# Optimization experiments

Hardware: AMD Instinct MI355X
Metric: run time of the kernel (lower is better)

## Reference

```python
import jax, jax.numpy as jnp
import numpy as np


def setup_inputs() -> dict:
    key = jax.random.key(0)
    ks = jax.random.split(key, 8)
    B, L, d_model = 2, 4096, 1024
    d_inner, d_state, d_conv, dt_rank = 2048, 16, 4, 64
    f = jnp.float32
    g = lambda k, shape, scale: jax.random.normal(k, shape, dtype=f) * scale
    # dt bias init: inverse-softplus of dt ~ U[log 1e-3, log 1e-1] (as in Mamba)
    dt = jnp.exp(jax.random.uniform(ks[5], (d_inner,), f) * (np.log(0.1) - np.log(0.001)) + np.log(0.001))
    dt = jnp.clip(dt, 1e-4, None)
    inv_dt = dt + jnp.log(-jnp.expm1(-dt))
    A_log = jnp.log(jnp.broadcast_to(jnp.arange(1, d_state + 1, dtype=f), (d_inner, d_state)))
    return {
        "hidden_states": jax.random.normal(ks[0], (B, L, d_model), f),
        "in_proj_w": g(ks[1], (2 * d_inner, d_model), 0.02),
        "conv_w": g(ks[2], (d_inner, d_conv), 0.1),
        "conv_b": jnp.zeros((d_inner,), f),
        "x_proj_w": g(ks[3], (dt_rank + 2 * d_state, d_inner), 0.02),
        "dt_proj_w": g(ks[4], (d_inner, dt_rank), dt_rank ** -0.5),
        "dt_proj_b": inv_dt,
        "A_log": A_log,
        "D": jnp.ones((d_inner,), f),
        "out_proj_w": g(ks[6], (d_model, d_inner), 0.02),
    }


def reference(hidden_states, in_proj_w, conv_w, conv_b, x_proj_w, dt_proj_w, dt_proj_b, A_log, D, out_proj_w):
    B_, L, _ = hidden_states.shape
    d_inner, d_conv = conv_w.shape
    dt_rank = dt_proj_w.shape[1]
    d_state = A_log.shape[1]

    # input projection -> x, z gates (B, L, d_inner) each
    xz = jnp.einsum('bld,ed->ble', hidden_states, in_proj_w)
    x, z = jnp.split(xz, 2, axis=-1)

    # causal depthwise conv1d over time + SiLU
    xc = jnp.transpose(x, (0, 2, 1))                       # (B, d_inner, L)
    kern = conv_w[:, None, :]                              # (O=d_inner, I/g=1, W)
    xc = jax.lax.conv_general_dilated(
        xc, kern, window_strides=(1,), padding=[(d_conv - 1, 0)],
        dimension_numbers=('NCH', 'OIH', 'NCH'), feature_group_count=d_inner)
    xc = xc + conv_b[None, :, None]
    x = jax.nn.silu(jnp.transpose(xc, (0, 2, 1)))          # (B, L, d_inner)

    # data-dependent SSM parameters
    x_dbl = jnp.einsum('bld,kd->blk', x, x_proj_w)         # (B, L, dt_rank+2n)
    dt, Bm, Cm = jnp.split(x_dbl, [dt_rank, dt_rank + d_state], axis=-1)
    dt = jnp.einsum('blr,dr->bld', dt, dt_proj_w)
    dt = jax.nn.softplus(dt + dt_proj_b)                   # delta_softplus + delta_bias
    A = -jnp.exp(A_log)                                    # (d_inner, d_state)

    # selective scan over the sequence dim; carry h: (B, d_inner, d_state)
    def step(h, inp):
        x_t, dt_t, B_t, C_t = inp                          # (B,d) (B,d) (B,n) (B,n)
        dA = jnp.exp(dt_t[..., None] * A)                  # (B, d, n)
        h = h * dA + (dt_t * x_t)[..., None] * B_t[:, None, :]
        y = jnp.einsum('bdn,bn->bd', h, C_t)
        return h, y

    h0 = jnp.zeros((B_, d_inner, d_state), x.dtype)
    xs = (jnp.transpose(x, (1, 0, 2)), jnp.transpose(dt, (1, 0, 2)),
          jnp.transpose(Bm, (1, 0, 2)), jnp.transpose(Cm, (1, 0, 2)))
    _, ys = jax.lax.scan(step, h0, xs)                     # ys: (L, B, d_inner)

    y = jnp.transpose(ys, (1, 0, 2)) + x * D               # skip via D
    y = y * jax.nn.silu(z)                                 # gate
    return jnp.einsum('bld,od->blo', y, out_proj_w)        # (B, L, d_model)
```

## Files before the change

kernel.cpp:

```cpp
#include <hip/hip_runtime.h>
#include <cmath>

#define CH 64
#define NC 64

typedef __bf16 bf16_t;
typedef __attribute__((ext_vector_type(8))) __bf16 bf16x8;
typedef __attribute__((ext_vector_type(4))) __bf16 bf16x4;
typedef __attribute__((ext_vector_type(4))) float f32x4;

#define GLOAD_LDS16(gp, lp)                                                     \
    __builtin_amdgcn_global_load_lds(                                           \
        (const __attribute__((address_space(1))) unsigned int*)(uintptr_t)(gp), \
        (__attribute__((address_space(3))) unsigned int*)(uintptr_t)(lp),       \
        16, 0, 0)

__global__ __launch_bounds__(256) void split5n(
    const float* __restrict__ a, bf16_t* __restrict__ ah, int n4a,
    const float* __restrict__ b, bf16_t* __restrict__ bh, int n4b,
    const float* __restrict__ c, bf16_t* __restrict__ ch, bf16_t* __restrict__ cl, int n4c,
    const float* __restrict__ d, bf16_t* __restrict__ dh, bf16_t* __restrict__ dl, int n4d,
    const float* __restrict__ e, bf16_t* __restrict__ eh, int n4e)
{
    int i = blockIdx.x * 256 + threadIdx.x;
    if (i < n4a) {
        const float4 v = ((const float4*)a)[i];
        bf16x4 hv = {(bf16_t)v.x, (bf16_t)v.y, (bf16_t)v.z, (bf16_t)v.w};
        ((bf16x4*)ah)[i] = hv;
        return;
    }
    i -= n4a;
    if (i < n4b) {
        const float4 v = ((const float4*)b)[i];
        bf16x4 hv = {(bf16_t)v.x, (bf16_t)v.y, (bf16_t)v.z, (bf16_t)v.w};
        ((bf16x4*)bh)[i] = hv;
        return;
    }
    i -= n4b;
    if (i >= n4c + n4d) {
        i -= n4c + n4d;
        if (i < n4e) {
            const float4 v = ((const float4*)e)[i];
            bf16x4 hv = {(bf16_t)v.x, (bf16_t)v.y, (bf16_t)v.z, (bf16_t)v.w};
            ((bf16x4*)eh)[i] = hv;
        }
        return;
    }
    const float* src; bf16_t* hp; bf16_t* lp;
    if (i < n4c) { src = c; hp = ch; lp = cl; }
    else         { i -= n4c; src = d; hp = dh; lp = dl; }

    const float4 v = ((const float4*)src)[i];
    const bf16_t h0 = (bf16_t)v.x, h1 = (bf16_t)v.y,
                 h2 = (bf16_t)v.z, h3 = (bf16_t)v.w;
    bf16x4 hv = {h0, h1, h2, h3};
    bf16x4 lv = {(bf16_t)(v.x - (float)h0), (bf16_t)(v.y - (float)h1),
                 (bf16_t)(v.z - (float)h2), (bf16_t)(v.w - (float)h3)};
    ((bf16x4*)hp)[i] = hv;
    ((bf16x4*)lp)[i] = lv;
}

__global__ __launch_bounds__(256) void add2(
    const float* __restrict__ a, const float* __restrict__ b,
    float* __restrict__ o, int n4)
{
    const int i = blockIdx.x * 256 + threadIdx.x;
    if (i >= n4) return;
    const float4 va = ((const float4*)a)[i];
    const float4 vb = ((const float4*)b)[i];
    ((float4*)o)[i] = make_float4(va.x + vb.x, va.y + vb.y,
                                  va.z + vb.z, va.w + vb.w);
}

__global__ __launch_bounds__(256) void add8_split(
    const float* __restrict__ p, float* __restrict__ o,
    bf16_t* __restrict__ dth, bf16_t* __restrict__ dtl,
    int n4, size_t stride4)
{
    const int i = blockIdx.x * 256 + threadIdx.x;
    if (i >= n4) return;
    float4 s = make_float4(0.f, 0.f, 0.f, 0.f);
#pragma unroll
    for (int k = 0; k < 8; ++k) {
        const float4 v = ((const float4*)p)[(size_t)k * stride4 + i];
        s.x += v.x; s.y += v.y; s.z += v.z; s.w += v.w;
    }
    ((float4*)o)[i] = s;

    const int col4 = i % 24;
    if (col4 < 16) {
        const int row = i / 24;
        const bf16_t h0 = (bf16_t)s.x, h1 = (bf16_t)s.y,
                     h2 = (bf16_t)s.z, h3 = (bf16_t)s.w;
        bf16x4 hv = {h0, h1, h2, h3};
        bf16x4 lv = {(bf16_t)(s.x - (float)h0), (bf16_t)(s.y - (float)h1),
                     (bf16_t)(s.z - (float)h2), (bf16_t)(s.w - (float)h3)};
        ((bf16x4*)dth)[(size_t)row * 16 + col4] = hv;
        ((bf16x4*)dtl)[(size_t)row * 16 + col4] = lv;
    }
}

__global__ __launch_bounds__(256) void in_proj_fused1(
    const bf16_t* __restrict__ Ah, const bf16_t* __restrict__ Wh,
    bf16_t* __restrict__ X, bf16_t* __restrict__ Z, int Ktot)
{
    __shared__ __align__(16) bf16_t Ash[128 * 32];
    __shared__ __align__(16) bf16_t Bsh[128 * 32];

    const int tid  = threadIdx.x;
    const int lane = tid & 63;
    const int w    = tid >> 6;
    const int wr   = (w >> 1) * 64;
    const int wc   = (w & 1) * 64;
    const int bm   = blockIdx.x * 128;
    const int by   = blockIdx.y;
    const int bnW  = by * 128;
    const int l16  = lane & 15;
    const int lhi  = lane >> 4;

    f32x4 acc[4][4];
#pragma unroll
    for (int i = 0; i < 4; ++i)
#pragma unroll
        for (int j = 0; j < 4; ++j)
#pragma unroll
            for (int r = 0; r < 4; ++r) acc[i][j][r] = 0.f;

    const int srow0 = tid >> 2;
    const int sks   = (tid & 3) << 3;
    const int ldsb0 = tid * 16;

    for (int k0 = 0; k0 < Ktot; k0 += 32) {
        __syncthreads();
#pragma unroll
        for (int call = 0; call < 2; ++call) {
            const int row = srow0 + call * 64;
            const int wb  = ldsb0 + call * 4096;
            GLOAD_LDS16(Ah + (size_t)(bm + row) * Ktot + k0 + sks, (char*)Ash + wb);
            GLOAD_LDS16(Wh + (size_t)(bnW + row) * Ktot + k0 + sks, (char*)Bsh + wb);
        }
        __syncthreads();

        bf16x8 af[4], bfr[4];
#pragma unroll
        for (int f = 0; f < 4; ++f) {
            af[f]  = *(const bf16x8*)&Ash[(wr + f * 16 + l16) * 32 + lhi * 8];
            bfr[f] = *(const bf16x8*)&Bsh[(wc + f * 16 + l16) * 32 + lhi * 8];
        }
#pragma unroll
        for (int fm = 0; fm < 4; ++fm)
#pragma unroll
            for (int fn = 0; fn < 4; ++fn)
                acc[fm][fn] = __builtin_amdgcn_mfma_f32_16x16x32_bf16(
                    af[fm], bfr[fn], acc[fm][fn], 0, 0, 0);
    }

    bf16_t* outp = (by < 16) ? X : Z;
    const int bnC = ((by < 16) ? by : (by - 16)) * 128;
#pragma unroll
    for (int fm = 0; fm < 4; ++fm) {
        const int row0 = bm + wr + fm * 16 + lhi * 4;
#pragma unroll
        for (int fn = 0; fn < 4; ++fn) {
            const int col = bnC + wc + fn * 16 + l16;
#pragma unroll
            for (int r = 0; r < 4; ++r)
                outp[(size_t)(row0 + r) * 2048 + col] = (bf16_t)acc[fm][fn][r];
        }
    }
}

template<int EPI>
__global__ __launch_bounds__(256) void gemm_mfma3p(
    const bf16_t* __restrict__ Ah, const bf16_t* __restrict__ Al,
    const bf16_t* __restrict__ Bh, const bf16_t* __restrict__ Bl,
    float* __restrict__ C, const float* __restrict__ bias,
    int Ktot, int ldc)
{
    __shared__ __align__(16) bf16_t Ash[128 * 32];
    __shared__ __align__(16) bf16_t Asl[128 * 32];
    __shared__ __align__(16) bf16_t Bsh[128 * 32];
    __shared__ __align__(16) bf16_t Bsl[128 * 32];

    const int tid  = threadIdx.x;
    const int lane = tid & 63;
    const int w    = tid >> 6;
    const int wr   = (w >> 1) * 64;
    const int wc   = (w & 1) * 64;
    const int bm   = blockIdx.x * 128;
    const int bn   = blockIdx.y * 128;
    const int l16  = lane & 15;
    const int lhi  = lane >> 4;

    f32x4 acc[4][4];
#pragma unroll
    for (int i = 0; i < 4; ++i)
#pragma unroll
        for (int j = 0; j < 4; ++j)
#pragma unroll
            for (int r = 0; r < 4; ++r) acc[i][j][r] = 0.f;

    const int srow0 = tid >> 2;
    const int sks   = (tid & 3) << 3;
    const int ldsb0 = tid * 16;

    for (int k0 = 0; k0 < Ktot; k0 += 32) {
        __syncthreads();
#pragma unroll
        for (int call = 0; call < 2; ++call) {
            const int row = srow0 + call * 64;
            const int wb  = ldsb0 + call * 4096;
            const size_t aoff = (size_t)(bm + row) * Ktot + k0 + sks;
            const size_t boff = (size_t)(bn + row) * Ktot + k0 + sks;
            GLOAD_LDS16(Ah + aoff, (char*)Ash + wb);
            GLOAD_LDS16(Al + aoff, (char*)Asl + wb);
            GLOAD_LDS16(Bh + boff, (char*)Bsh + wb);
            GLOAD_LDS16(Bl + boff, (char*)Bsl + wb);
        }
        __syncthreads();

        bf16x8 ah[4], al[4], bh[4], bl[4];
#pragma unroll
        for (int f = 0; f < 4; ++f) {
            const int ar = (wr + f * 16 + l16) * 32 + lhi * 8;
            const int br = (wc + f * 16 + l16) * 32 + lhi * 8;
            ah[f] = *(const bf16x8*)&Ash[ar];
            al[f] = *(const bf16x8*)&Asl[ar];
            bh[f] = *(const bf16x8*)&Bsh[br];
            bl[f] = *(const bf16x8*)&Bsl[br];
        }
#pragma unroll
        for (int fm = 0; fm < 4; ++fm)
#pragma unroll
            for (int fn = 0; fn < 4; ++fn) {
                acc[fm][fn] = __builtin_amdgcn_mfma_f32_16x16x32_bf16(
                    ah[fm], bh[fn], acc[fm][fn], 0, 0, 0);
                acc[fm][fn] = __builtin_amdgcn_mfma_f32_16x16x32_bf16(
                    al[fm], bh[fn], acc[fm][fn], 0, 0, 0);
                acc[fm][fn] = __builtin_amdgcn_mfma_f32_16x16x32_bf16(
                    ah[fm], bl[fn], acc[fm][fn], 0, 0, 0);
            }
    }

#pragma unroll
    for (int fm = 0; fm < 4; ++fm) {
        const int row0 = bm + wr + fm * 16 + lhi * 4;
#pragma unroll
        for (int fn = 0; fn < 4; ++fn) {
            const int col = bn + wc + fn * 16 + l16;
#pragma unroll
            for (int r = 0; r < 4; ++r) {
                float v = acc[fm][fn][r];
                const size_t m = row0 + r;
                if (EPI == 2) {
                    v += bias[col];
                    v = (v > 20.f) ? v : log1pf(expf(v));
                }
                C[m * ldc + col] = v;
            }
        }
    }
}

__global__ __launch_bounds__(256) void gemm_mfma3x(
    const bf16_t* __restrict__ Ah, const bf16_t* __restrict__ Al,
    const bf16_t* __restrict__ Bh, const bf16_t* __restrict__ Bl,
    float* __restrict__ C, int Ktot, int Ksplit, size_t partStride)
{
    __shared__ __align__(16) bf16_t Ash[128 * 32];
    __shared__ __align__(16) bf16_t Asl[128 * 32];
    __shared__ __align__(16) bf16_t Bsh[128 * 32];
    __shared__ __align__(16) bf16_t Bsl[128 * 32];

    const int tid  = threadIdx.x;
    const int lane = tid & 63;
    const int w    = tid >> 6;
    const int wr   = (w >> 1) * 64;
    const int wc   = (w & 1) * 64;
    const int bm   = blockIdx.x * 128;
    const int l16  = lane & 15;
    const int lhi  = lane >> 4;

    f32x4 acc[4][4];
#pragma unroll
    for (int i = 0; i < 4; ++i)
#pragma unroll
        for (int j = 0; j < 4; ++j)
#pragma unroll
            for (int r = 0; r < 4; ++r) acc[i][j][r] = 0.f;

    const int srow0 = tid >> 2;
    const int sks   = (tid & 3) << 3;
    const int ldsb0 = tid * 16;

    const int kBeg = blockIdx.z * Ksplit;
    const int kEnd = kBeg + Ksplit;

    for (int k0 = kBeg; k0 < kEnd; k0 += 32) {
        __syncthreads();
#pragma unroll
        for (int call = 0; call < 2; ++call) {
            const int row  = srow0 + call * 64;
            const int brow = (row < 96) ? row : 95;
            const int wb   = ldsb0 + call * 4096;
            const size_t aoff = (size_t)(bm + row) * Ktot + k0 + sks;
            const size_t boff = (size_t)brow * Ktot + k0 + sks;
            GLOAD_LDS16(Ah + aoff, (char*)Ash + wb);
            GLOAD_LDS16(Al + aoff, (char*)Asl + wb);
            GLOAD_LDS16(Bh + boff, (char*)Bsh + wb);
            GLOAD_LDS16(Bl + boff, (char*)Bsl + wb);
        }
        __syncthreads();

        bf16x8 ah[4], al[4], bh[4], bl[4];
#pragma unroll
        for (int f = 0; f < 4; ++f) {
            const int ar = (wr + f * 16 + l16) * 32 + lhi * 8;
            const int br = (wc + f * 16 + l16) * 32 + lhi * 8;
            ah[f] = *(const bf16x8*)&Ash[ar];
            al[f] = *(const bf16x8*)&Asl[ar];
            bh[f] = *(const bf16x8*)&Bsh[br];
            bl[f] = *(const bf16x8*)&Bsl[br];
        }
#pragma unroll
        for (int fm = 0; fm < 4; ++fm)
#pragma unroll
            for (int fn = 0; fn < 4; ++fn) {
                acc[fm][fn] = __builtin_amdgcn_mfma_f32_16x16x32_bf16(
                    ah[fm], bh[fn], acc[fm][fn], 0, 0, 0);
                acc[fm][fn] = __builtin_amdgcn_mfma_f32_16x16x32_bf16(
                    al[fm], bh[fn], acc[fm][fn], 0, 0, 0);
                acc[fm][fn] = __builtin_amdgcn_mfma_f32_16x16x32_bf16(
                    ah[fm], bl[fn], acc[fm][fn], 0, 0, 0);
            }
    }

    float* Cp = C + (size_t)blockIdx.z * partStride;
#pragma unroll
    for (int fm = 0; fm < 4; ++fm) {
        const int row0 = bm + wr + fm * 16 + lhi * 4;
#pragma unroll
        for (int fn = 0; fn < 4; ++fn) {
            const int col = wc + fn * 16 + l16;
            if (col < 96) {
#pragma unroll
                for (int r = 0; r < 4; ++r)
                    Cp[(size_t)(row0 + r) * 96 + col] = acc[fm][fn][r];
            }
        }
    }
}

__global__ __launch_bounds__(256) void gemm_mfma1o128sk(
    const bf16_t* __restrict__ Ah, const bf16_t* __restrict__ Bh,
    float* __restrict__ C, int K, int Ksplit, int ldc, size_t partStride)
{
    __shared__ __align__(16) bf16_t Ash[128 * 32];
    __shared__ __align__(16) bf16_t Bsh[128 * 32];

    const int tid  = threadIdx.x;
    const int lane = tid & 63;
    const int w    = tid >> 6;
    const int wr   = (w >> 1) * 64;
    const int wc   = (w & 1) * 64;
    const int bm   = blockIdx.x * 128;
    const int bn   = blockIdx.y * 128;
    const int l16  = lane & 15;
    const int lhi  = lane >> 4;

    f32x4 acc[4][4];
#pragma unroll
    for (int i = 0; i < 4; ++i)
#pragma unroll
        for (int j = 0; j < 4; ++j)
#pragma unroll
            for (int r = 0; r < 4; ++r) acc[i][j][r] = 0.f;

    const int srow0 = tid >> 2;
    const int sks   = (tid & 3) << 3;
    const int ldsb0 = tid * 16;

    const int kBeg = blockIdx.z * Ksplit;
    const int kEnd = kBeg + Ksplit;

    for (int k0 = kBeg; k0 < kEnd; k0 += 32) {
        __syncthreads();
#pragma unroll
        for (int call = 0; call < 2; ++call) {
            const int row = srow0 + call * 64;
            const int wb  = ldsb0 + call * 4096;
            GLOAD_LDS16(Ah + (size_t)(bm + row) * K + k0 + sks, (char*)Ash + wb);
            GLOAD_LDS16(Bh + (size_t)(bn + row) * K + k0 + sks, (char*)Bsh + wb);
        }
        __syncthreads();

        bf16x8 af[4], bfr[4];
#pragma unroll
        for (int f = 0; f < 4; ++f) {
            af[f]  = *(const bf16x8*)&Ash[(wr + f * 16 + l16) * 32 + lhi * 8];
            bfr[f] = *(const bf16x8*)&Bsh[(wc + f * 16 + l16) * 32 + lhi * 8];
        }
#pragma unroll
        for (int fm = 0; fm < 4; ++fm)
#pragma unroll
            for (int fn = 0; fn < 4; ++fn)
                acc[fm][fn] = __builtin_amdgcn_mfma_f32_16x16x32_bf16(
                    af[fm], bfr[fn], acc[fm][fn], 0, 0, 0);
    }

    float* Cp = C + (size_t)blockIdx.z * partStride;
#pragma unroll
    for (int fm = 0; fm < 4; ++fm) {
        const int row0 = bm + wr + fm * 16 + lhi * 4;
#pragma unroll
        for (int fn = 0; fn < 4; ++fn) {
            const int col = bn + wc + fn * 16 + l16;
#pragma unroll
            for (int r = 0; r < 4; ++r)
                Cp[(size_t)(row0 + r) * ldc + col] = acc[fm][fn][r];
        }
    }
}

__global__ __launch_bounds__(256) void conv_silu8b(
    const bf16_t* __restrict__ xin, const float* __restrict__ w,
    const float* __restrict__ bias,
    bf16_t* __restrict__ xh, bf16_t* __restrict__ xl,
    int L, int D)
{
    const long long e8 = (long long)blockIdx.x * 256 + threadIdx.x;
    const int Dq = D >> 3;
    const int dq = (int)(e8 % Dq);
    const long long bl = e8 / Dq;
    const int l = (int)(bl % L);
    const int d = dq << 3;
    const long long base = bl * D + d;

    float t0[8], t1[8], t2[8], t3[8];
    {
        const bf16x8 v = *(const bf16x8*)&xin[base];
#pragma unroll
        for (int j = 0; j < 8; ++j) t0[j] = (float)v[j];
    }
    if (l >= 1) { const bf16x8 v = *(const bf16x8*)&xin[base - D];
#pragma unroll
        for (int j = 0; j < 8; ++j) t1[j] = (float)v[j];
    } else { for (int j = 0; j < 8; ++j) t1[j] = 0.f; }
    if (l >= 2) { const bf16x8 v = *(const bf16x8*)&xin[base - 2 * D];
#pragma unroll
        for (int j = 0; j < 8; ++j) t2[j] = (float)v[j];
    } else { for (int j = 0; j < 8; ++j) t2[j] = 0.f; }
    if (l >= 3) { const bf16x8 v = *(const bf16x8*)&xin[base - 3 * D];
#pragma unroll
        for (int j = 0; j < 8; ++j) t3[j] = (float)v[j];
    } else { for (int j = 0; j < 8; ++j) t3[j] = 0.f; }

    bf16x8 hv, lv;
#pragma unroll
    for (int j = 0; j < 8; ++j) {
        const float4 wv = *(const float4*)&w[(d + j) * 4];
        float acc = bias[d + j];
        acc = fmaf(wv.w, t0[j], acc);
        acc = fmaf(wv.z, t1[j], acc);
        acc = fmaf(wv.y, t2[j], acc);
        acc = fmaf(wv.x, t3[j], acc);
        const float o = acc / (1.f + __expf(-acc));
        const bf16_t h = (bf16_t)o;
        hv[j] = h;
        lv[j] = (bf16_t)(o - (float)h);
    }
    *(bf16x8*)&xh[base] = hv;
    *(bf16x8*)&xl[base] = lv;
}

__global__ __launch_bounds__(256) void scan_local2(
    const bf16_t* __restrict__ xh, const bf16_t* __restrict__ xl,
    const float* __restrict__ dt,
    const float* __restrict__ xdbl,  const float* __restrict__ A_log,
    float* __restrict__ Sbuf, float* __restrict__ Pbuf)
{
    __shared__ float Bs[CH][16];

    const int d = blockIdx.x * 256 + threadIdx.x;
    const int c = blockIdx.y;
    const int b = blockIdx.z;
    const long long rowBase = (long long)b * 4096 + (long long)c * CH;

    {
        const int e = threadIdx.x;
        const int i = e >> 2, j = (e & 3) << 2;
        *(float4*)&Bs[i][j] = *(const float4*)&xdbl[(rowBase + i) * 96 + 64 + j];
    }
    __syncthreads();

    float a[16], S[16];
#pragma unroll
    for (int n = 0; n < 16; ++n) {
        a[n] = -__expf(A_log[d * 16 + n]);
        S[n] = 0.f;
    }
    float sumdt = 0.f;

    for (int i = 0; i < CH; ++i) {
        const long long row = rowBase + i;
        const float dtv = dt[row * 2048 + d];
        const float xv  = (float)xh[row * 2048 + d] + (float)xl[row * 2048 + d];
        const float u   = dtv * xv;
        sumdt += dtv;
#pragma unroll
        for (int n = 0; n < 16; ++n) {
            const float dA = __expf(dtv * a[n]);
            S[n] = fmaf(S[n], dA, u * Bs[i][n]);
        }
    }

    const size_t base = ((((size_t)b * NC + c) * 2048) + d) * 16;
#pragma unroll
    for (int k = 0; k < 4; ++k) {
        *(float4*)&Sbuf[base + k * 4] =
            make_float4(S[k*4], S[k*4+1], S[k*4+2], S[k*4+3]);
        *(float4*)&Pbuf[base + k * 4] =
            make_float4(__expf(sumdt * a[k*4]),   __expf(sumdt * a[k*4+1]),
                        __expf(sumdt * a[k*4+2]), __expf(sumdt * a[k*4+3]));
    }
}

__global__ __launch_bounds__(256) void scan_chunk_prefix(
    float* __restrict__ Sbuf, const float* __restrict__ Pbuf)
{
    const int tid = blockIdx.x * 256 + threadIdx.x;
    const int b  = tid >> 15;
    const int dn = tid & 32767;

    float H = 0.f;
    for (int c = 0; c < NC; ++c) {
        const size_t idx = ((size_t)b * NC + c) * 32768 + dn;
        const float S = Sbuf[idx];
        const float P = Pbuf[idx];
        Sbuf[idx] = H;
        H = fmaf(P, H, S);
    }
}

__global__ __launch_bounds__(256) void scan_final2(
    const bf16_t* __restrict__ xh, const bf16_t* __restrict__ xl,
    const float* __restrict__ dt,
    const float* __restrict__ xdbl,  const float* __restrict__ A_log,
    const float* __restrict__ Dp,    const bf16_t* __restrict__ z,
    const float* __restrict__ Hbuf,  bf16_t* __restrict__ y)
{
    __shared__ float BCs[CH][32];

    const int d = blockIdx.x * 256 + threadIdx.x;
    const int c = blockIdx.y;
    const int b = blockIdx.z;
    const long long rowBase = (long long)b * 4096 + (long long)c * CH;

#pragma unroll
    for (int k = 0; k < 2; ++k) {
        const int e = k * 256 + threadIdx.x;
        const int i = e >> 3, j = (e & 7) << 2;
        *(float4*)&BCs[i][j] = *(const float4*)&xdbl[(rowBase + i) * 96 + 64 + j];
    }
    __syncthreads();

    float a[16], h[16];
    const size_t hbase = ((((size_t)b * NC + c) * 2048) + d) * 16;
#pragma unroll
    for (int k = 0; k < 4; ++k) {
        const float4 hv = *(const float4*)&Hbuf[hbase + k * 4];
        h[k*4] = hv.x; h[k*4+1] = hv.y; h[k*4+2] = hv.z; h[k*4+3] = hv.w;
    }
#pragma unroll
    for (int n = 0; n < 16; ++n) a[n] = -__expf(A_log[d * 16 + n]);
    const float Dv = Dp[d];

    for (int i = 0; i < CH; ++i) {
        const long long row = rowBase + i;
        const float dtv = dt[row * 2048 + d];
        const float xv  = (float)xh[row * 2048 + d] + (float)xl[row * 2048 + d];
        const float u   = dtv * xv;
        float acc = 0.f;
#pragma unroll
        for (int n = 0; n < 16; ++n) {
            const float dA = __expf(dtv * a[n]);
            h[n] = fmaf(h[n], dA, u * BCs[i][n]);
            acc  = fmaf(h[n], BCs[i][16 + n], acc);
        }
        const float zv = (float)z[row * 2048 + d];
        float yv = acc + xv * Dv;
        yv = yv * (zv / (1.f + __expf(-zv)));
        y[row * 2048 + d] = (bf16_t)yv;
    }
}

extern "C" void kernel_launch(void* const* d_in, const int* in_sizes, int n_in,
                              void* d_out, int out_size, void* d_ws, size_t ws_size,
                              hipStream_t stream)
{
    const float* hidden     = (const float*)d_in[0];
    const float* in_proj_w  = (const float*)d_in[1];
    const float* conv_w     = (const float*)d_in[2];
    const float* conv_b     = (const float*)d_in[3];
    const float* x_proj_w   = (const float*)d_in[4];
    const float* dt_proj_w  = (const float*)d_in[5];
    const float* dt_proj_b  = (const float*)d_in[6];
    const float* A_log      = (const float*)d_in[7];
    const float* Dvec       = (const float*)d_in[8];
    const float* out_proj_w = (const float*)d_in[9];
    float* out = (float*)d_out;

    const int L = 4096, dinner = 2048, dmodel = 1024;
    const int M = 2 * L;

    float* z     = (float*)d_ws;
    float* xraw  = z     + (size_t)M * dinner;
    float* xconv = xraw  + (size_t)M * dinner;
    float* xdbl  = xconv + (size_t)M * dinner;
    float* Sbuf  = xdbl  + (size_t)M * 96;

    bf16_t* w1_h  = (bf16_t*)Sbuf;
    bf16_t* hid_h = (bf16_t*)xconv;
    bf16_t* zb    = (bf16_t*)z;
    bf16_t* Xb    = (bf16_t*)xraw;
    bf16_t* xc_h  = (bf16_t*)xconv;
    bf16_t* xc_l  = xc_h + (size_t)M * dinner;
    float*  xp_part = xraw;
    bf16_t* dth  = (bf16_t*)Sbuf;
    bf16_t* dtl  = dth + (size_t)M * 64;
    bf16_t* wdh  = (bf16_t*)out;
    bf16_t* wdl  = wdh + (size_t)dinner * 64;
    bf16_t* xpwh = (bf16_t*)xdbl;
    bf16_t* xpwl = xpwh + (size_t)96 * dinner;
    bf16_t* w2_h = zb + (size_t)M * dinner;
    float*  Pbuf = (float*)(w2_h + (size_t)dmodel * dinner);
    float*  op_part = xraw;

    const int n4a = M * dmodel / 4;
    const int n4b = 2 * dinner * dmodel / 4;
    const int n4c = dinner * 64 / 4;
    const int n4d = 96 * dinner / 4;
    const int n4e = dmodel * dinner / 4;
    split5n<<<(n4a + n4b + n4c + n4d + n4e + 255) / 256, 256, 0, stream>>>(
        hidden, hid_h, n4a,
        in_proj_w, w1_h, n4b,
        dt_proj_w, wdh, wdl, n4c,
        x_proj_w, xpwh, xpwl, n4d,
        out_proj_w, w2_h, n4e);

    in_proj_fused1<<<dim3(M / 128, 32), 256, 0, stream>>>(
        hid_h, w1_h, Xb, zb, dmodel);

    conv_silu8b<<<(M * (long long)dinner / 8) / 256, 256, 0, stream>>>(
        Xb, conv_w, conv_b, xc_h, xc_l, L, dinner);

    gemm_mfma3x<<<dim3(M / 128, 1, 8), 256, 0, stream>>>(
        xc_h, xc_l, xpwh, xpwl, xp_part, dinner, dinner / 8, (size_t)M * 96);
    add8_split<<<(M * 96 / 4 + 255) / 256, 256, 0, stream>>>(
        xp_part, xdbl, dth, dtl, M * 96 / 4, (size_t)M * 96 / 4);

    gemm_mfma3p<2><<<dim3(M / 128, 2048 / 128), 256, 0, stream>>>(
        dth, dtl, wdh, wdl, xraw, dt_proj_b, 64, 2048);

    scan_local2<<<dim3(dinner / 256, NC, 2), 256, 0, stream>>>(
        xc_h, xc_l, xraw, xdbl, A_log, Sbuf, Pbuf);
    scan_chunk_prefix<<<256, 256, 0, stream>>>(Sbuf, Pbuf);
    scan_final2<<<dim3(dinner / 256, NC, 2), 256, 0, stream>>>(
        xc_h, xc_l, xraw, xdbl, A_log, Dvec, zb, Sbuf, xc_h);

    gemm_mfma1o128sk<<<dim3(M / 128, 1024 / 128, 2), 256, 0, stream>>>(
        xc_h, w2_h, op_part, dinner, dinner / 2, 1024, (size_t)M * 1024);
    add2<<<(M * dmodel / 4 + 255) / 256, 256, 0, stream>>>(
        op_part, op_part + (size_t)M * 1024, out, M * dmodel / 4);
}
```

Measured before the change: 463.4 us.

## Store dt as bf16 and reduce out_proj split-K with atomics into output

The dt projection epilogue now writes softplus(dt) as bf16 rather than fp32, which halves the dt traffic that both scan kernels read. The out_proj split-K GEMM now zeroes the output with a memset and atomically adds its two partial products into it, which removes the fp32 partial buffers and the separate add kernel. The cost is reduced precision in dt, which feeds the exponent of the scan, plus atomic-add contention and a memset launch.

Measured after the change: 480.1 us. 1.04x slower.

```diff
diff --git a/kernel.cpp b/kernel.cpp
--- a/kernel.cpp
+++ b/kernel.cpp
@@ -58,18 +58,6 @@
                  (bf16_t)(v.z - (float)h2), (bf16_t)(v.w - (float)h3)};
     ((bf16x4*)hp)[i] = hv;
     ((bf16x4*)lp)[i] = lv;
-}
-
-__global__ __launch_bounds__(256) void add2(
-    const float* __restrict__ a, const float* __restrict__ b,
-    float* __restrict__ o, int n4)
-{
-    const int i = blockIdx.x * 256 + threadIdx.x;
-    if (i >= n4) return;
-    const float4 va = ((const float4*)a)[i];
-    const float4 vb = ((const float4*)b)[i];
-    ((float4*)o)[i] = make_float4(va.x + vb.x, va.y + vb.y,
-                                  va.z + vb.z, va.w + vb.w);
 }
 
 __global__ __launch_bounds__(256) void add8_split(
@@ -170,11 +158,10 @@
     }
 }
 
-template<int EPI>
-__global__ __launch_bounds__(256) void gemm_mfma3p(
+__global__ __launch_bounds__(256) void gemm_mfma3dt(
     const bf16_t* __restrict__ Ah, const bf16_t* __restrict__ Al,
     const bf16_t* __restrict__ Bh, const bf16_t* __restrict__ Bl,
-    float* __restrict__ C, const float* __restrict__ bias,
+    bf16_t* __restrict__ C, const float* __restrict__ bias,
     int Ktot, int ldc)
 {
     __shared__ __align__(16) bf16_t Ash[128 * 32];
@@ -250,13 +237,9 @@
             const int col = bn + wc + fn * 16 + l16;
 #pragma unroll
             for (int r = 0; r < 4; ++r) {
-                float v = acc[fm][fn][r];
-                const size_t m = row0 + r;
-                if (EPI == 2) {
-                    v += bias[col];
-                    v = (v > 20.f) ? v : log1pf(expf(v));
-                }
-                C[m * ldc + col] = v;
+                float v = acc[fm][fn][r] + bias[col];
+                v = (v > 20.f) ? v : log1pf(expf(v));
+                C[(size_t)(row0 + r) * ldc + col] = (bf16_t)v;
             }
         }
     }
@@ -351,9 +334,9 @@
     }
 }
 
-__global__ __launch_bounds__(256) void gemm_mfma1o128sk(
+__global__ __launch_bounds__(256) void gemm_mfma1o128at(
     const bf16_t* __restrict__ Ah, const bf16_t* __restrict__ Bh,
-    float* __restrict__ C, int K, int Ksplit, int ldc, size_t partStride)
+    float* __restrict__ C, int K, int Ksplit, int ldc)
 {
     __shared__ __align__(16) bf16_t Ash[128 * 32];
     __shared__ __align__(16) bf16_t Bsh[128 * 32];
@@ -408,7 +391,6 @@
                     af[fm], bfr[fn], acc[fm][fn], 0, 0, 0);
     }
 
-    float* Cp = C + (size_t)blockIdx.z * partStride;
 #pragma unroll
     for (int fm = 0; fm < 4; ++fm) {
         const int row0 = bm + wr + fm * 16 + lhi * 4;
@@ -417,7 +399,7 @@
             const int col = bn + wc + fn * 16 + l16;
 #pragma unroll
             for (int r = 0; r < 4; ++r)
-                Cp[(size_t)(row0 + r) * ldc + col] = acc[fm][fn][r];
+                atomicAdd(&C[(size_t)(row0 + r) * ldc + col], acc[fm][fn][r]);
         }
     }
 }
@@ -475,7 +457,7 @@
 
 __global__ __launch_bounds__(256) void scan_local2(
     const bf16_t* __restrict__ xh, const bf16_t* __restrict__ xl,
-    const float* __restrict__ dt,
+    const bf16_t* __restrict__ dtb,
     const float* __restrict__ xdbl,  const float* __restrict__ A_log,
     float* __restrict__ Sbuf, float* __restrict__ Pbuf)
 {
@@ -503,7 +485,7 @@
 
     for (int i = 0; i < CH; ++i) {
         const long long row = rowBase + i;
-        const float dtv = dt[row * 2048 + d];
+        const float dtv = (float)dtb[row * 2048 + d];
         const float xv  = (float)xh[row * 2048 + d] + (float)xl[row * 2048 + d];
         const float u   = dtv * xv;
         sumdt += dtv;
@@ -544,7 +526,7 @@
 
 __global__ __launch_bounds__(256) void scan_final2(
     const bf16_t* __restrict__ xh, const bf16_t* __restrict__ xl,
-    const float* __restrict__ dt,
+    const bf16_t* __restrict__ dtb,
     const float* __restrict__ xdbl,  const float* __restrict__ A_log,
     const float* __restrict__ Dp,    const bf16_t* __restrict__ z,
     const float* __restrict__ Hbuf,  bf16_t* __restrict__ y)
@@ -577,7 +559,7 @@
 
     for (int i = 0; i < CH; ++i) {
         const long long row = rowBase + i;
-        const float dtv = dt[row * 2048 + d];
+        const float dtv = (float)dtb[row * 2048 + d];
         const float xv  = (float)xh[row * 2048 + d] + (float)xl[row * 2048 + d];
         const float u   = dtv * xv;
         float acc = 0.f;
@@ -626,6 +608,7 @@
     bf16_t* xc_h  = (bf16_t*)xconv;
     bf16_t* xc_l  = xc_h + (size_t)M * dinner;
     float*  xp_part = xraw;
+    bf16_t* dtb  = (bf16_t*)xraw;
     bf16_t* dth  = (bf16_t*)Sbuf;
     bf16_t* dtl  = dth + (size_t)M * 64;
     bf16_t* wdh  = (bf16_t*)out;
@@ -634,7 +617,6 @@
     bf16_t* xpwl = xpwh + (size_t)96 * dinner;
     bf16_t* w2_h = zb + (size_t)M * dinner;
     float*  Pbuf = (float*)(w2_h + (size_t)dmodel * dinner);
-    float*  op_part = xraw;
 
     const int n4a = M * dmodel / 4;
     const int n4b = 2 * dinner * dmodel / 4;
@@ -659,17 +641,16 @@
     add8_split<<<(M * 96 / 4 + 255) / 256, 256, 0, stream>>>(
         xp_part, xdbl, dth, dtl, M * 96 / 4, (size_t)M * 96 / 4);
 
-    gemm_mfma3p<2><<<dim3(M / 128, 2048 / 128), 256, 0, stream>>>(
-        dth, dtl, wdh, wdl, xraw, dt_proj_b, 64, 2048);
+    gemm_mfma3dt<<<dim3(M / 128, 2048 / 128), 256, 0, stream>>>(
+        dth, dtl, wdh, wdl, dtb, dt_proj_b, 64, 2048);
 
     scan_local2<<<dim3(dinner / 256, NC, 2), 256, 0, stream>>>(
-        xc_h, xc_l, xraw, xdbl, A_log, Sbuf, Pbuf);
+        xc_h, xc_l, dtb, xdbl, A_log, Sbuf, Pbuf);
     scan_chunk_prefix<<<256, 256, 0, stream>>>(Sbuf, Pbuf);
     scan_final2<<<dim3(dinner / 256, NC, 2), 256, 0, stream>>>(
-        xc_h, xc_l, xraw, xdbl, A_log, Dvec, zb, Sbuf, xc_h);
-
-    gemm_mfma1o128sk<<<dim3(M / 128, 1024 / 128, 2), 256, 0, stream>>>(
-        xc_h, w2_h, op_part, dinner, dinner / 2, 1024, (size_t)M * 1024);
-    add2<<<(M * dmodel / 4 + 255) / 256, 256, 0, stream>>>(
-        op_part, op_part + (size_t)M * 1024, out, M * dmodel / 4);
-}
+        xc_h, xc_l, dtb, xdbl, A_log, Dvec, zb, Sbuf, xc_h);
+
+    hipMemsetAsync(out, 0, (size_t)M * dmodel * sizeof(float), stream);
+    gemm_mfma1o128at<<<dim3(M / 128, 1024 / 128, 2), 256, 0, stream>>>(
+        xc_h, w2_h, out, dinner, dinner / 2, 1024);
+}
```
